# Performance work log

Measured on AMD Instinct MI355X. Metric: run time of the kernel, lower is better.

The kernel has to match this reference:

```python
import jax, jax.numpy as jnp
import numpy as np

DIM = 512
HEADS = 8
DH = DIM // HEADS          # 64
M = DIM // 2               # 256 landmarks
PINV_ITERS = 6
KERNEL = 33                # residual_conv_kernel (lucidrains default)
SCALE = DH ** -0.5
LN_EPS = 1e-5


def setup_inputs() -> dict:
    key = jax.random.key(0)
    ks = jax.random.split(key, 6)
    b, n = 4, 4096
    x = jax.random.normal(ks[0], (b, n, DIM), jnp.float32)
    ln_w = jnp.ones((DIM,), jnp.float32)
    ln_b = jnp.zeros((DIM,), jnp.float32)
    w_qkv = jax.random.normal(ks[1], (DIM, 3 * DIM), jnp.float32) / np.float32(np.sqrt(DIM))
    w_out = jax.random.normal(ks[2], (DIM, DIM), jnp.float32) / np.float32(np.sqrt(DIM))
    b_out = jnp.zeros((DIM,), jnp.float32)
    # depthwise Conv2d(heads, heads, (33,1), groups=heads, bias=False): OIHW = (8,1,33,1)
    conv_w = jax.random.normal(ks[3], (HEADS, 1, KERNEL, 1), jnp.float32) / np.float32(np.sqrt(KERNEL))
    # admin_torch.as_module(8): residual x*omega + f(x), omega learnable scalar init sqrt(8)
    omega = jnp.asarray(np.sqrt(8.0), jnp.float32)
    return dict(x=x, ln_w=ln_w, ln_b=ln_b, w_qkv=w_qkv, w_out=w_out,
                b_out=b_out, conv_w=conv_w, omega=omega)


def _layernorm(x, w, b):
    mu = x.mean(-1, keepdims=True)
    var = x.var(-1, keepdims=True)
    return (x - mu) * jax.lax.rsqrt(var + LN_EPS) * w + b


def _moore_penrose_pinv(x, iters):
    # Newton-Schulz iteration, exactly as lucidrains nystrom-attention
    abs_x = jnp.abs(x)
    col = abs_x.sum(-1)
    row = abs_x.sum(-2)
    z = jnp.swapaxes(x, -1, -2) / (jnp.max(col) * jnp.max(row))
    I = jnp.eye(x.shape[-1], dtype=x.dtype)
    for _ in range(iters):
        xz = x @ z
        z = 0.25 * z @ (13. * I - xz @ (15. * I - xz @ (7. * I - xz)))
    return z


def reference(x, ln_w, ln_b, w_qkv, w_out, b_out, conv_w, omega):
    b, n, _ = x.shape
    nx = _layernorm(x, ln_w, ln_b)
    qkv = nx @ w_qkv                                # [b, n, 3*dim]
    q, k, v = jnp.split(qkv, 3, axis=-1)
    to_heads = lambda t: t.reshape(b, n, HEADS, DH).transpose(0, 2, 1, 3)  # bhnd
    q = to_heads(q) * SCALE
    k = to_heads(k)
    v = to_heads(v)
    l = n // M                                      # tokens per landmark group
    q_l = q.reshape(b, HEADS, M, l, DH).mean(3)     # [b,h,m,d]
    k_l = k.reshape(b, HEADS, M, l, DH).mean(3)
    sim1 = jnp.einsum('bhid,bhjd->bhij', q, k_l)    # [b,h,n,m]
    sim2 = jnp.einsum('bhid,bhjd->bhij', q_l, k_l)  # [b,h,m,m]
    sim3 = jnp.einsum('bhid,bhjd->bhij', q_l, k)    # [b,h,m,n]
    a1 = jax.nn.softmax(sim1, -1)
    a2 = jax.nn.softmax(sim2, -1)
    a3 = jax.nn.softmax(sim3, -1)
    a2_inv = _moore_penrose_pinv(a2, PINV_ITERS)
    out = (a1 @ a2_inv) @ (a3 @ v)                  # [b,h,n,d]
    # residual depthwise conv along the sequence dim of v
    res = jax.lax.conv_general_dilated(
        v, conv_w, window_strides=(1, 1),
        padding=((KERNEL // 2, KERNEL // 2), (0, 0)),
        dimension_numbers=('NCHW', 'OIHW', 'NCHW'),
        feature_group_count=HEADS)
    out = out + res
    out = out.transpose(0, 2, 1, 3).reshape(b, n, HEADS * DH)
    out = out @ w_out + b_out                       # to_out (dropout is eval no-op)
    return x * omega + out                          # admin residual
```

## Files before the change

### kernel.cpp

```cpp
#include <hip/hip_runtime.h>
#include <math.h>

#define B_    4
#define N_    4096
#define DIM_  512
#define H_    8
#define DH_   64
#define M_    256
#define LGRP  16
#define BH_   (B_*H_)
#define SCALE_ 0.125f
#define LN_EPS_ 1e-5f

#define SZ_QKVH (B_*H_*N_*DH_)
#define SZ_LM   (BH_*M_*DH_)
#define SZ_MM   (BH_*M_*M_)

typedef unsigned short ushort_t;
typedef __attribute__((ext_vector_type(8))) short bfrag8;
typedef __attribute__((ext_vector_type(4))) float fvec4;

__device__ __forceinline__ ushort_t f2b(float f) {
    unsigned u = __float_as_uint(f);
    unsigned r = (u + 0x7fffu + ((u >> 16) & 1u)) >> 16;
    return (ushort_t)r;
}
__device__ __forceinline__ float b2f(ushort_t s) {
    return __uint_as_float(((unsigned)s) << 16);
}

__device__ __forceinline__ void gload16(const ushort_t* g, ushort_t* l) {
    __builtin_amdgcn_global_load_lds(
        (const __attribute__((address_space(1))) void*)g,
        (__attribute__((address_space(3))) void*)l, 16, 0, 0);
}

__global__ __launch_bounds__(256) void ln_kernel(const float* __restrict__ x,
                                                 const float* __restrict__ w,
                                                 const float* __restrict__ bb,
                                                 ushort_t* __restrict__ nxb) {
    int row = blockIdx.x;
    int t = threadIdx.x;
    const float* xr = x + (size_t)row * DIM_;
    float v0 = xr[t], v1 = xr[t + 256];
    float s = v0 + v1, sq = v0 * v0 + v1 * v1;
    __shared__ float ls[4], lq[4];
    for (int off = 32; off > 0; off >>= 1) {
        s  += __shfl_down(s, off);
        sq += __shfl_down(sq, off);
    }
    int wid = t >> 6, lid = t & 63;
    if (lid == 0) { ls[wid] = s; lq[wid] = sq; }
    __syncthreads();
    if (t == 0) {
        float S = 0, Q = 0;
        for (int i = 0; i < 4; i++) { S += ls[i]; Q += lq[i]; }
        ls[0] = S; lq[0] = Q;
    }
    __syncthreads();
    float mean = ls[0] * (1.f / DIM_);
    float var  = lq[0] * (1.f / DIM_) - mean * mean;
    float rs = rsqrtf(var + LN_EPS_);
    ushort_t* o = nxb + (size_t)row * DIM_;
    o[t]       = f2b((v0 - mean) * rs * w[t]       + bb[t]);
    o[t + 256] = f2b((v1 - mean) * rs * w[t + 256] + bb[t + 256]);
}

__global__ __launch_bounds__(256) void tcast(const float* __restrict__ in,
                                             ushort_t* __restrict__ outT,
                                             int R, int C) {
    __shared__ float tile[32][33];
    int c0 = blockIdx.x * 32, r0 = blockIdx.y * 32;
    int t = threadIdx.x;
    #pragma unroll
    for (int u = 0; u < 4; u++) {
        int lin = t + 256 * u;
        int r = lin >> 5, c = lin & 31;
        tile[r][c] = in[(size_t)(r0 + r) * C + c0 + c];
    }
    __syncthreads();
    #pragma unroll
    for (int u = 0; u < 4; u++) {
        int lin = t + 256 * u;
        int cc = lin >> 5, rr = lin & 31;
        outT[(size_t)(c0 + cc) * R + r0 + rr] = f2b(tile[rr][cc]);
    }
}

template<int EPI>
__global__ __launch_bounds__(256) void gemm_bt128(const ushort_t* __restrict__ A,
                                                  const ushort_t* __restrict__ BT,
                                                  ushort_t* __restrict__ qb,
                                                  ushort_t* __restrict__ kb,
                                                  ushort_t* __restrict__ vb,
                                                  const float* __restrict__ x,
                                                  const float* __restrict__ bo,
                                                  const float* __restrict__ omega,
                                                  float* __restrict__ out) {
    const int K = 512;
    __shared__ __align__(16) ushort_t smem[4 * 128 * 64];
    int t = threadIdx.x;
    int lin = blockIdx.x + blockIdx.y * gridDim.x;
    int nwg = gridDim.x * gridDim.y;
    int wg  = (lin & 7) * (nwg >> 3) + (lin >> 3);
    int n0 = (wg % gridDim.x) * 128, m0 = (wg / gridDim.x) * 128;
    int w = t >> 6, lane = t & 63;
    int wr = (w >> 1) * 64, wc = (w & 1) * 64;
    int l15 = lane & 15, quad = lane >> 4, kq = quad * 8;
    int lrow = lane >> 3, lc8 = (lane & 7) * 8;
    fvec4 acc[4][4] = {};

    auto stage = [&](int buf, int kc) {
        ushort_t* Ad = smem + buf * 16384;
        ushort_t* Bd = Ad + 8192;
        #pragma unroll
        for (int u = 0; u < 4; u++) {
            int r0 = (w << 5) + (u << 3);
            int row = r0 + lrow;
            const ushort_t* ga;
            if (EPI == 0) {
                ga = A + (size_t)(m0 + row) * K + kc + lc8;
            } else {
                int grow = m0 + row; int b_ = grow >> 12, nn = grow & 4095;
                ga = A + (((size_t)(b_ * H_ + (kc >> 6)) * N_ + nn) << 6) + lc8;
            }
            gload16(ga, Ad + r0 * 64);
            gload16(BT + (size_t)(n0 + row) * K + kc + lc8, Bd + r0 * 64);
        }
    };

    stage(0, 0);
    __syncthreads();
    int cur = 0;
    for (int kt = 0; kt < 8; ++kt) {
        if (kt < 7) stage(cur ^ 1, (kt + 1) * 64);
        const ushort_t* As = smem + cur * 16384;
        const ushort_t* Bs = As + 8192;
        #pragma unroll
        for (int ks = 0; ks < 64; ks += 32) {
            bfrag8 a[4], b[4];
            #pragma unroll
            for (int r = 0; r < 4; r++) a[r] = *(bfrag8*)(As + (wr + r * 16 + l15) * 64 + ks + kq);
            #pragma unroll
            for (int c = 0; c < 4; c++) b[c] = *(bfrag8*)(Bs + (wc + c * 16 + l15) * 64 + ks + kq);
            #pragma unroll
            for (int r = 0; r < 4; r++)
                #pragma unroll
                for (int c = 0; c < 4; c++)
                    acc[r][c] = __builtin_amdgcn_mfma_f32_16x16x32_bf16(a[r], b[c], acc[r][c], 0, 0, 0);
        }
        __syncthreads();
        cur ^= 1;
    }

    if (EPI == 0) {
        int sec = n0 >> 9;
        float mul = (sec == 0) ? SCALE_ : 1.0f;
        ushort_t (*Ct)[132] = (ushort_t(*)[132])smem;
        #pragma unroll
        for (int r = 0; r < 4; r++) {
            #pragma unroll
            for (int reg = 0; reg < 4; reg++) {
                int lr = wr + r * 16 + quad * 4 + reg;
                #pragma unroll
                for (int c = 0; c < 4; c++) {
                    int lc = wc + c * 16 + l15;
                    Ct[lr][lc] = f2b(acc[r][c][reg] * mul);
                }
            }
        }
        __syncthreads();
        int row = t & 127, half = t >> 7;
        int grow = m0 + row; int b_ = grow >> 12, nn = grow & 4095;
        int head = ((n0 & 511) >> 6) + half;
        ushort_t* dstbuf = (sec == 0) ? qb : ((sec == 1) ? kb : vb);
        ushort_t* dp = dstbuf + (((size_t)(b_ * H_ + head) * N_ + nn) << 6);
        #pragma unroll
        for (int i = 0; i < 8; i++)
            *(uint4*)(dp + i * 8) = *(uint4*)&Ct[row][half * 64 + i * 8];
    } else {
        float om = omega[0];
        #pragma unroll
        for (int r = 0; r < 4; r++) {
            #pragma unroll
            for (int reg = 0; reg < 4; reg++) {
                int grow = m0 + wr + r * 16 + quad * 4 + reg;
                #pragma unroll
                for (int c = 0; c < 4; c++) {
                    int gcol = n0 + wc + c * 16 + l15;
                    size_t o = (size_t)grow * DIM_ + gcol;
                    out[o] = om * x[o] + bo[gcol] + acc[r][c][reg];
                }
            }
        }
    }
}

__global__ __launch_bounds__(256) void landmark_kernel(const ushort_t* __restrict__ q,
                                                       const ushort_t* __restrict__ k,
                                                       ushort_t* __restrict__ ql,
                                                       ushort_t* __restrict__ kl) {
    int idx = blockIdx.x * 256 + threadIdx.x;
    const ushort_t* src = blockIdx.y ? k : q;
    ushort_t* dst = blockIdx.y ? kl : ql;
    int d8 = (idx & 7) * 8;
    int m = (idx >> 3) & 255;
    int bh = idx >> 11;
    const ushort_t* p = src + (((size_t)bh * N_) + m * LGRP) * DH_ + d8;
    float s[8] = {};
    #pragma unroll
    for (int j = 0; j < LGRP; j++) {
        union { uint4 u4; ushort_t sv[8]; } val;
        val.u4 = *(const uint4*)(p + (size_t)j * DH_);
        #pragma unroll
        for (int e = 0; e < 8; e++) s[e] += b2f(val.sv[e]);
    }
    union { uint4 u4; ushort_t sv[8]; } o;
    #pragma unroll
    for (int e = 0; e < 8; e++) o.sv[e] = f2b(s[e] * (1.f / LGRP));
    *(uint4*)(dst + ((size_t)bh * M_ + m) * DH_ + d8) = o.u4;
}

__global__ __launch_bounds__(256) void sim2_softmax(const ushort_t* __restrict__ ql,
                                                    const ushort_t* __restrict__ kl,
                                                    float* __restrict__ a2,
                                                    ushort_t* __restrict__ a2b) {
    int i = blockIdx.x, bh = blockIdx.y, j = threadIdx.x;
    __shared__ float qrow[64];
    __shared__ float red[256];
    if (j < 64) qrow[j] = b2f(ql[((size_t)bh * M_ + i) * DH_ + j]);
    __syncthreads();
    const ushort_t* kr = kl + ((size_t)bh * M_ + j) * DH_;
    float s = 0;
    #pragma unroll
    for (int d = 0; d < 64; d++) s += qrow[d] * b2f(kr[d]);
    red[j] = s; __syncthreads();
    for (int off = 128; off > 0; off >>= 1) {
        if (j < off) red[j] = fmaxf(red[j], red[j + off]);
        __syncthreads();
    }
    float mx = red[0]; __syncthreads();
    float p = __expf(s - mx);
    red[j] = p; __syncthreads();
    for (int off = 128; off > 0; off >>= 1) {
        if (j < off) red[j] += red[j + off];
        __syncthreads();
    }
    float res = p / red[0];
    size_t o = ((size_t)bh * M_ + i) * M_ + j;
    a2[o] = res;
    a2b[o] = f2b(res);
}

__global__ void zero2(unsigned* p) { if (threadIdx.x < 2) p[threadIdx.x] = 0u; }

__global__ __launch_bounds__(256) void colpart(const float* __restrict__ a2,
                                               float* __restrict__ cs2) {
    int bh = blockIdx.x, s = blockIdx.y, t = threadIdx.x;
    const float* A = a2 + ((size_t)bh << 16) + (size_t)s * 32 * M_;
    float cs = 0.f;
    #pragma unroll
    for (int i = 0; i < 32; i++) cs += A[(size_t)i * M_ + t];
    cs2[((size_t)s * BH_ + bh) * M_ + t] = cs;
}

__global__ __launch_bounds__(256) void colmax(const float* __restrict__ cs2, unsigned* red) {
    int bh = blockIdx.x, t = threadIdx.x;
    float v = 0.f;
    #pragma unroll
    for (int s = 0; s < 8; s++) v += cs2[((size_t)s * BH_ + bh) * M_ + t];
    __shared__ float lr[256];
    lr[t] = v; __syncthreads();
    for (int off = 128; off > 0; off >>= 1) {
        if (t < off) lr[t] = fmaxf(lr[t], lr[t + off]);
        __syncthreads();
    }
    if (t == 0) atomicMax(red, __float_as_uint(lr[0]));
}

__global__ __launch_bounds__(256) void pinv_init2(const float* __restrict__ a2,
                                                  const unsigned* __restrict__ red,
                                                  ushort_t* __restrict__ zA,
                                                  ushort_t* __restrict__ zAT) {
    __shared__ float tile[32][33];
    int bt = blockIdx.z; int j0 = blockIdx.x * 32, i0 = blockIdx.y * 32;
    float invd = 1.f / __uint_as_float(red[0]);
    const float* Ab = a2 + ((size_t)bt << 16);
    size_t bo = (size_t)bt << 16;
    int t = threadIdx.x;
    #pragma unroll
    for (int u = 0; u < 4; u++) {
        int lin = t + 256 * u; int r = lin >> 5, c = lin & 31;
        float vv = Ab[(size_t)(i0 + r) * M_ + j0 + c] * invd;
        tile[r][c] = vv;
        zAT[bo + (size_t)(i0 + r) * M_ + j0 + c] = f2b(vv);
    }
    __syncthreads();
    #pragma unroll
    for (int u = 0; u < 4; u++) {
        int lin = t + 256 * u; int cc = lin >> 5, rr = lin & 31;
        zA[bo + (size_t)(j0 + cc) * M_ + i0 + rr] = f2b(tile[rr][cc]);
    }
}

__global__ __launch_bounds__(256) void gemm_pinv(const ushort_t* __restrict__ A,
                                                 const ushort_t* __restrict__ BT,
                                                 ushort_t* __restrict__ outN,
                                                 ushort_t* __restrict__ outT,
                                                 ushort_t* __restrict__ outT1,
                                                 float* __restrict__ outF,
                                                 float coefI, float scale) {
    __shared__ __align__(16) ushort_t smem[2 * 8192];
    int t = threadIdx.x;
    int lin = blockIdx.x + (blockIdx.y << 2) + (blockIdx.z << 4);
    int wg  = (lin & 7) * 64 + (lin >> 3);
    int n0 = (wg & 3) * 64, m0 = ((wg >> 2) & 3) * 64;
    int bt = wg >> 4;
    const ushort_t* Ab = A + ((size_t)bt << 16);
    const ushort_t* Bb = BT + ((size_t)bt << 16);
    int w = t >> 6, lane = t & 63;
    int wr = (w >> 1) * 32, wc = (w & 1) * 32;
    int l15 = lane & 15, quad = lane >> 4, kq = quad * 8;
    int lrow = lane >> 3, lc8 = (lane & 7) * 8;
    fvec4 acc[2][2] = {};

    auto stage = [&](int buf, int kc) {
        ushort_t* Ad = smem + buf * 8192;
        ushort_t* Bd = Ad + 4096;
        #pragma unroll
        for (int u = 0; u < 2; u++) {
            int r0 = (w << 4) + (u << 3);
            int row = r0 + lrow;
            gload16(Ab + (size_t)(m0 + row) * M_ + kc + lc8, Ad + r0 * 64);
            gload16(Bb + (size_t)(n0 + row) * M_ + kc + lc8, Bd + r0 * 64);
        }
    };

    stage(0, 0);
    __syncthreads();
    int cur = 0;
    for (int kt = 0; kt < 4; ++kt) {
        if (kt < 3) stage(cur ^ 1, (kt + 1) * 64);
        const ushort_t* As = smem + cur * 8192;
        const ushort_t* Bs = As + 4096;
        #pragma unroll
        for (int ks = 0; ks < 64; ks += 32) {
            bfrag8 a[2], b[2];
            #pragma unroll
            for (int r = 0; r < 2; r++) a[r] = *(bfrag8*)(As + (wr + r * 16 + l15) * 64 + ks + kq);
            #pragma unroll
            for (int c = 0; c < 2; c++) b[c] = *(bfrag8*)(Bs + (wc + c * 16 + l15) * 64 + ks + kq);
            #pragma unroll
            for (int r = 0; r < 2; r++)
                #pragma unroll
                for (int c = 0; c < 2; c++)
                    acc[r][c] = __builtin_amdgcn_mfma_f32_16x16x32_bf16(a[r], b[c], acc[r][c], 0, 0, 0);
        }
        __syncthreads();
        cur ^= 1;
    }

    size_t bto = (size_t)bt << 16;
    if (outN || outF) {
        #pragma unroll
        for (int r = 0; r < 2; r++) {
            #pragma unroll
            for (int reg = 0; reg < 4; reg++) {
                int grow = m0 + wr + r * 16 + quad * 4 + reg;
                #pragma unroll
                for (int c = 0; c < 2; c++) {
                    int gcol = n0 + wc + c * 16 + l15;
                    float cv = scale * acc[r][c][reg] + (grow == gcol ? coefI : 0.f);
                    if (outN) outN[bto + (size_t)grow * M_ + gcol] = f2b(cv);
                    if (outF) outF[bto + (size_t)grow * M_ + gcol] = cv;
                }
            }
        }
    }
    if (outT || outT1) {
        ushort_t (*Ct)[65] = (ushort_t(*)[65])&smem[0];
        #pragma unroll
        for (int r = 0; r < 2; r++) {
            #pragma unroll
            for (int reg = 0; reg < 4; reg++) {
                int lr = wr + r * 16 + quad * 4 + reg;
                #pragma unroll
                for (int c = 0; c < 2; c++) {
                    int lc = wc + c * 16 + l15;
                    float cv = scale * acc[r][c][reg] + ((m0 + lr) == (n0 + lc) ? coefI : 0.f);
                    Ct[lr][lc] = f2b(cv);
                }
            }
        }
        __syncthreads();
        int j = t & 63, quarter = t >> 6, i0 = quarter * 16;
        #pragma unroll
        for (int vq = 0; vq < 2; vq++) {
            union { uint4 u4; ushort_t s[8]; } o1, o2;
            #pragma unroll
            for (int e = 0; e < 8; e++) {
                int il = i0 + vq * 8 + e;
                ushort_t bv = Ct[il][j];
                o1.s[e] = bv;
                o2.s[e] = f2b(((m0 + il) == (n0 + j) ? 7.f : 0.f) - b2f(bv));
            }
            size_t dst = bto + (size_t)(n0 + j) * M_ + m0 + i0 + vq * 8;
            if (outT)  *(uint4*)&outT[dst]  = o1.u4;
            if (outT1) *(uint4*)&outT1[dst] = o2.u4;
        }
    }
}

template<int NCH, int TRANSV>
__global__ __launch_bounds__(256) void flash_mfma(const ushort_t* __restrict__ Q,
                                                  const ushort_t* __restrict__ K,
                                                  const ushort_t* __restrict__ V,
                                                  ushort_t* __restrict__ Obf,
                                                  float* __restrict__ Opart,
                                                  float* __restrict__ lout,
                                                  int nq, int nk) {
    int bh = blockIdx.y;
    int nqt = nq >> 6;
    int qt = blockIdx.x % nqt;
    int ch = blockIdx.x / nqt;
    int q0 = qt * 64;
    int chunk = nk / NCH;
    int j0 = ch * chunk, j1 = j0 + chunk;

    __shared__ __align__(16) ushort_t qs[64][72];
    __shared__ __align__(16) ushort_t ks[64][72];
    __shared__ __align__(16) ushort_t vts[64][72];
    __shared__ __align__(16) ushort_t pb[64][72];

    int t = threadIdx.x;
    int w = t >> 6, lane = t & 63;
    int l15 = lane & 15, quad = lane >> 4, kq = quad * 8;
    int wrow = w * 16;

    const ushort_t* Qb = Q + ((size_t)bh * nq + q0) * DH_;
    #pragma unroll
    for (int u = 0; u < 2; u++) {
        int lin = t + 256 * u;
        int r = lin >> 3, cc = (lin & 7) * 8;
        *(uint4*)&qs[r][cc] = *(const uint4*)(Qb + r * DH_ + cc);
    }

    fvec4 Oacc[4];
    #pragma unroll
    for (int nt = 0; nt < 4; nt++)
        #pragma unroll
        for (int reg = 0; reg < 4; reg++) Oacc[nt][reg] = 0.f;
    float l_[4] = {0.f, 0.f, 0.f, 0.f};

    const ushort_t* VTbase = V + (size_t)bh * DH_ * nk;

    uint4 kreg[2], vreg[2];
    auto loadkv = [&](int j) {
        const ushort_t* Kb = K + ((size_t)bh * nk + j) * DH_;
        #pragma unroll
        for (int u = 0; u < 2; u++) {
            int lin = t + 256 * u;
            int r = lin >> 3, cc = (lin & 7) * 8;
            kreg[u] = *(const uint4*)(Kb + r * DH_ + cc);
            if (TRANSV == 0)
                vreg[u] = *(const uint4*)(VTbase + (size_t)r * nk + j + cc);
            else
                vreg[u] = *(const uint4*)(V + ((size_t)(bh * nk + j + r)) * DH_ + cc);
        }
    };
    auto writekv = [&]() {
        #pragma unroll
        for (int u = 0; u < 2; u++) {
            int lin = t + 256 * u;
            int r = lin >> 3, cc = (lin & 7) * 8;
            *(uint4*)&ks[r][cc] = kreg[u];
            if (TRANSV == 0) {
                *(uint4*)&vts[r][cc] = vreg[u];
            } else {
                union { uint4 u4; ushort_t s[8]; } vv;
                vv.u4 = vreg[u];
                #pragma unroll
                for (int m = 0; m < 8; m++) vts[cc + m][r] = vv.s[m];
            }
        }
    };

    loadkv(j0);
    for (int j = j0; j < j1; j += 64) {
        writekv();
        __syncthreads();
        if (j + 64 < j1) loadkv(j + 64);

        fvec4 S[4];
        #pragma unroll
        for (int ct = 0; ct < 4; ct++)
            #pragma unroll
            for (int reg = 0; reg < 4; reg++) S[ct][reg] = 0.f;
        bfrag8 aq0 = *(bfrag8*)&qs[wrow + l15][kq];
        bfrag8 aq1 = *(bfrag8*)&qs[wrow + l15][32 + kq];
        #pragma unroll
        for (int ct = 0; ct < 4; ct++) {
            bfrag8 b0 = *(bfrag8*)&ks[ct * 16 + l15][kq];
            bfrag8 b1 = *(bfrag8*)&ks[ct * 16 + l15][32 + kq];
            S[ct] = __builtin_amdgcn_mfma_f32_16x16x32_bf16(aq0, b0, S[ct], 0, 0, 0);
            S[ct] = __builtin_amdgcn_mfma_f32_16x16x32_bf16(aq1, b1, S[ct], 0, 0, 0);
        }

        float ps[4] = {0.f, 0.f, 0.f, 0.f};
        #pragma unroll
        for (int ct = 0; ct < 4; ct++) {
            #pragma unroll
            for (int reg = 0; reg < 4; reg++) {
                float pv = __expf(S[ct][reg]);
                ps[reg] += pv;
                pb[wrow + quad * 4 + reg][ct * 16 + l15] = f2b(pv);
            }
        }
        #pragma unroll
        for (int reg = 0; reg < 4; reg++) {
            float s = ps[reg];
            s += __shfl_xor(s, 1);
            s += __shfl_xor(s, 2);
            s += __shfl_xor(s, 4);
            s += __shfl_xor(s, 8);
            l_[reg] += s;
        }

        bfrag8 ap0 = *(bfrag8*)&pb[wrow + l15][kq];
        bfrag8 ap1 = *(bfrag8*)&pb[wrow + l15][32 + kq];
        #pragma unroll
        for (int nt = 0; nt < 4; nt++) {
            bfrag8 b0 = *(bfrag8*)&vts[nt * 16 + l15][kq];
            bfrag8 b1 = *(bfrag8*)&vts[nt * 16 + l15][32 + kq];
            Oacc[nt] = __builtin_amdgcn_mfma_f32_16x16x32_bf16(ap0, b0, Oacc[nt], 0, 0, 0);
            Oacc[nt] = __builtin_amdgcn_mfma_f32_16x16x32_bf16(ap1, b1, Oacc[nt], 0, 0, 0);
        }
        __syncthreads();
    }

    if (NCH == 1) {
        #pragma unroll
        for (int reg = 0; reg < 4; reg++) {
            float inv = 1.f / l_[reg];
            #pragma unroll
            for (int nt = 0; nt < 4; nt++)
                qs[wrow + quad * 4 + reg][nt * 16 + l15] = f2b(Oacc[nt][reg] * inv);
        }
        __syncthreads();
        ushort_t* Ob = Obf + ((size_t)bh * nq + q0) * DH_;
        #pragma unroll
        for (int u = 0; u < 2; u++) {
            int lin = t + 256 * u;
            int r = lin >> 3, i = (lin & 7) * 8;
            *(uint4*)(Ob + (size_t)r * DH_ + i) = *(uint4*)&qs[r][i];
        }
    } else {
        size_t rows_per_ch = (size_t)BH_ * nq;
        #pragma unroll
        for (int reg = 0; reg < 4; reg++) {
            size_t rowg = (size_t)bh * nq + q0 + wrow + quad * 4 + reg;
            #pragma unroll
            for (int nt = 0; nt < 4; nt++)
                Opart[((size_t)ch * rows_per_ch + rowg) * DH_ + nt * 16 + l15] = Oacc[nt][reg];
            if (l15 == 0)
                lout[(size_t)ch * rows_per_ch + rowg] = l_[reg];
        }
    }
}

__global__ __launch_bounds__(256) void flash_combine(const float* __restrict__ apart,
                                                     const float* __restrict__ lpart,
                                                     ushort_t* __restrict__ a3vb) {
    int idx = blockIdx.x * 256 + threadIdx.x;
    int d = idx & 63; int row = idx >> 6;
    const int R = BH_ * M_;
    float l = lpart[row] + lpart[row + R] + lpart[row + 2 * R] + lpart[row + 3 * R];
    size_t e = (size_t)row * DH_ + d;
    const size_t CH = (size_t)R * DH_;
    float o = apart[e] + apart[e + CH] + apart[e + 2 * CH] + apart[e + 3 * CH];
    a3vb[e] = f2b(o / l);
}

__global__ __launch_bounds__(256) void wm_mfma(const ushort_t* __restrict__ Z,
                                               const ushort_t* __restrict__ A3V,
                                               ushort_t* __restrict__ WmT) {
    __shared__ __align__(16) ushort_t As[64][72];
    __shared__ __align__(16) ushort_t Bs[64][72];
    int bh = blockIdx.y;
    int i0 = blockIdx.x * 64;
    const ushort_t* Zb = Z + ((size_t)bh << 16);
    const ushort_t* Ab = A3V + ((size_t)bh << 14);
    int t = threadIdx.x;
    int w = t >> 6, lane = t & 63;
    int wr = (w >> 1) * 32, wc = (w & 1) * 32;
    int l15 = lane & 15, quad = lane >> 4, kq = quad * 8;
    fvec4 acc[2][2] = {};
    int rbase = t >> 3, c8 = (t & 7) * 8;

    for (int kc = 0; kc < M_; kc += 64) {
        #pragma unroll
        for (int u = 0; u < 2; u++) {
            int rr = rbase + 32 * u;
            *(float4*)&Bs[rr][c8] = *(const float4*)(Zb + (size_t)(i0 + rr) * M_ + kc + c8);
            union { uint4 u4; ushort_t s[8]; } av;
            av.u4 = *(const uint4*)(Ab + (size_t)(kc + rr) * DH_ + c8);
            #pragma unroll
            for (int m = 0; m < 8; m++) As[c8 + m][rr] = av.s[m];
        }
        __syncthreads();
        #pragma unroll
        for (int ks = 0; ks < 64; ks += 32) {
            bfrag8 a[2], b[2];
            #pragma unroll
            for (int r = 0; r < 2; r++) a[r] = *(bfrag8*)&As[wr + r * 16 + l15][ks + kq];
            #pragma unroll
            for (int c = 0; c < 2; c++) b[c] = *(bfrag8*)&Bs[wc + c * 16 + l15][ks + kq];
            #pragma unroll
            for (int r = 0; r < 2; r++)
                #pragma unroll
                for (int c = 0; c < 2; c++)
                    acc[r][c] = __builtin_amdgcn_mfma_f32_16x16x32_bf16(a[r], b[c], acc[r][c], 0, 0, 0);
        }
        __syncthreads();
    }
    #pragma unroll
    for (int r = 0; r < 2; r++) {
        #pragma unroll
        for (int reg = 0; reg < 4; reg++) {
            int drow = wr + r * 16 + quad * 4 + reg;
            ushort_t* dp = WmT + ((size_t)bh * DH_ + drow) * M_;
            #pragma unroll
            for (int c = 0; c < 2; c++)
                dp[i0 + wc + c * 16 + l15] = f2b(acc[r][c][reg]);
        }
    }
}

__global__ __launch_bounds__(256) void conv_kernel(const ushort_t* __restrict__ V,
                                                   const float* __restrict__ cw,
                                                   const ushort_t* __restrict__ ctxb,
                                                   ushort_t* __restrict__ outb) {
    int bh = blockIdx.y;
    int h = bh & 7;
    int i0 = blockIdx.x * 64;
    __shared__ float vb[96][64];
    __shared__ float wloc[33];
    int t = threadIdx.x;
    if (t < 33) wloc[t] = cw[h * 33 + t];
    #pragma unroll
    for (int u = 0; u < 3; u++) {
        int lin = t + 256 * u;
        int r = lin >> 3, cc = (lin & 7) * 8;
        int gi = i0 - 16 + r;
        union { uint4 u4; ushort_t s[8]; } val;
        if (gi >= 0 && gi < N_)
            val.u4 = *(const uint4*)(V + ((size_t)bh * N_ + gi) * DH_ + cc);
        else
            val.u4 = make_uint4(0, 0, 0, 0);
        #pragma unroll
        for (int m = 0; m < 8; m++) vb[r][cc + m] = b2f(val.s[m]);
    }
    __syncthreads();
    int d = t & 63, rb = t >> 6;
    for (int u = 0; u < 16; u++) {
        int r = rb * 16 + u;
        float s = 0.f;
        #pragma unroll
        for (int kk = 0; kk < 33; kk++) s += wloc[kk] * vb[r + kk][d];
        size_t o = ((size_t)bh * N_ + i0 + r) * DH_ + d;
        outb[o] = f2b(b2f(ctxb[o]) + s);
    }
}

extern "C" void kernel_launch(void* const* d_in, const int* in_sizes, int n_in,
                              void* d_out, int out_size, void* d_ws, size_t ws_size,
                              hipStream_t stream) {
    const float* x      = (const float*)d_in[0];
    const float* ln_w   = (const float*)d_in[1];
    const float* ln_b   = (const float*)d_in[2];
    const float* w_qkv  = (const float*)d_in[3];
    const float* w_out  = (const float*)d_in[4];
    const float* b_out  = (const float*)d_in[5];
    const float* conv_w = (const float*)d_in[6];
    const float* omega  = (const float*)d_in[7];
    float* out = (float*)d_out;

    float* fp = (float*)d_ws;
    float* a2    = fp;              fp += SZ_MM;
    float* apart = fp;              fp += SZ_QKVH / 4;
    float* lpart = fp;              fp += 4 * BH_ * M_;
    float* cs2   = fp;              fp += 8 * BH_ * M_;
    ushort_t* us = (ushort_t*)fp;
    ushort_t* wqkvT = us;           us += DIM_ * 3 * DIM_;
    ushort_t* woT   = us;           us += DIM_ * DIM_;
    ushort_t* a2b   = us;           us += SZ_MM;
    ushort_t* zA    = us;           us += SZ_MM;
    ushort_t* zAT   = us;           us += SZ_MM;
    ushort_t* zB    = us;           us += SZ_MM;
    ushort_t* zBT   = us;           us += SZ_MM;
    ushort_t* qb    = us;           us += SZ_QKVH;
    ushort_t* kb    = us;           us += SZ_QKVH;
    ushort_t* vb    = us;           us += SZ_QKVH;
    ushort_t* ctxb  = us;           us += SZ_QKVH;
    ushort_t* outhb = us;           us += SZ_QKVH;
    ushort_t* ql    = us;           us += SZ_LM;
    ushort_t* kl    = us;           us += SZ_LM;
    ushort_t* WmT   = us;           us += SZ_LM;
    ushort_t* a3vb  = us;           us += SZ_LM;
    unsigned* red   = (unsigned*)us;
    ushort_t* nxb = outhb;
    ushort_t* xz  = ctxb;
    ushort_t* t1T = xz  + SZ_MM;
    ushort_t* t2T = t1T + SZ_MM;
    ushort_t* t3T = t2T + SZ_MM;

    ln_kernel<<<B_ * N_, 256, 0, stream>>>(x, ln_w, ln_b, nxb);
    tcast<<<dim3(48, 16), 256, 0, stream>>>(w_qkv, wqkvT, DIM_, 3 * DIM_);
    tcast<<<dim3(16, 16), 256, 0, stream>>>(w_out, woT, DIM_, DIM_);
    gemm_bt128<0><<<dim3(12, 128), 256, 0, stream>>>(nxb, wqkvT, qb, kb, vb,
                                                     nullptr, nullptr, nullptr, nullptr);
    landmark_kernel<<<dim3(256, 2), 256, 0, stream>>>(qb, kb, ql, kl);
    sim2_softmax<<<dim3(M_, BH_), 256, 0, stream>>>(ql, kl, a2, a2b);
    zero2<<<1, 64, 0, stream>>>(red);
    colpart<<<dim3(BH_, 8), 256, 0, stream>>>(a2, cs2);
    colmax<<<BH_, 256, 0, stream>>>(cs2, red);
    pinv_init2<<<dim3(8, 8, 32), 256, 0, stream>>>(a2, red, zA, zAT);

    ushort_t* za = zA;  ushort_t* zaT = zAT;
    ushort_t* zb = zB;  ushort_t* zbT = zBT;
    for (int it = 0; it < 6; it++) {
        gemm_pinv<<<dim3(4, 4, BH_), 256, 0, stream>>>(a2b, zaT, xz, nullptr, t1T, nullptr, 0.f, 1.f);
        gemm_pinv<<<dim3(4, 4, BH_), 256, 0, stream>>>(xz, t1T, nullptr, t2T, nullptr, nullptr, 15.f, -1.f);
        gemm_pinv<<<dim3(4, 4, BH_), 256, 0, stream>>>(xz, t2T, nullptr, t3T, nullptr, nullptr, 13.f, -1.f);
        gemm_pinv<<<dim3(4, 4, BH_), 256, 0, stream>>>(za, t3T, zb, (it < 5) ? zbT : nullptr,
                                                       nullptr, nullptr, 0.f, 0.25f);
        ushort_t* tp;
        tp = za; za = zb; zb = tp;
        tp = zaT; zaT = zbT; zbT = tp;
    }

    flash_mfma<4, 1><<<dim3(16, BH_), 256, 0, stream>>>(ql, kb, vb, nullptr, apart, lpart, M_, N_);
    flash_combine<<<(BH_ * M_ * DH_) / 256, 256, 0, stream>>>(apart, lpart, a3vb);
    wm_mfma<<<dim3(4, BH_), 256, 0, stream>>>(za, a3vb, WmT);
    flash_mfma<1, 0><<<dim3(64, BH_), 256, 0, stream>>>(qb, kl, WmT, ctxb, nullptr, nullptr, N_, M_);
    conv_kernel<<<dim3(N_ / 64, BH_), 256, 0, stream>>>(vb, conv_w, ctxb, outhb);
    gemm_bt128<1><<<dim3(4, 128), 256, 0, stream>>>(outhb, woT, nullptr, nullptr, nullptr,
                                                    x, b_out, omega, out);
}
```

Before: 500.8 us.

## Swizzle GEMM shared-memory tiles, double split-K chunks, stage partial outputs via LDS

Applies an XOR swizzle to the LDS layout of the QKV/out-projection and pinv GEMM tiles so MFMA fragment reads avoid bank conflicts. Raises the a3·v flash split count from 4 to 8 chunks to launch more workgroups for the short-query path, with the combine kernel summing 8 partials. Partial outputs are now staged through shared memory and written as coalesced float4 stores. The extra chunks double partial-buffer traffic and combine work.

```diff
diff --git a/kernel.cpp b/kernel.cpp
--- a/kernel.cpp
+++ b/kernel.cpp
@@ -108,6 +108,8 @@
     int wr = (w >> 1) * 64, wc = (w & 1) * 64;
     int l15 = lane & 15, quad = lane >> 4, kq = quad * 8;
     int lrow = lane >> 3, lc8 = (lane & 7) * 8;
+    int scol = lc8 ^ ((lrow & 7) << 3);
+    int sw   = (l15 & 7) << 3;
     fvec4 acc[4][4] = {};
 
     auto stage = [&](int buf, int kc) {
@@ -119,13 +121,13 @@
             int row = r0 + lrow;
             const ushort_t* ga;
             if (EPI == 0) {
-                ga = A + (size_t)(m0 + row) * K + kc + lc8;
+                ga = A + (size_t)(m0 + row) * K + kc + scol;
             } else {
                 int grow = m0 + row; int b_ = grow >> 12, nn = grow & 4095;
-                ga = A + (((size_t)(b_ * H_ + (kc >> 6)) * N_ + nn) << 6) + lc8;
+                ga = A + (((size_t)(b_ * H_ + (kc >> 6)) * N_ + nn) << 6) + scol;
             }
             gload16(ga, Ad + r0 * 64);
-            gload16(BT + (size_t)(n0 + row) * K + kc + lc8, Bd + r0 * 64);
+            gload16(BT + (size_t)(n0 + row) * K + kc + scol, Bd + r0 * 64);
         }
     };
 
@@ -138,11 +140,12 @@
         const ushort_t* Bs = As + 8192;
         #pragma unroll
         for (int ks = 0; ks < 64; ks += 32) {
+            int kcol = (ks + kq) ^ sw;
             bfrag8 a[4], b[4];
             #pragma unroll
-            for (int r = 0; r < 4; r++) a[r] = *(bfrag8*)(As + (wr + r * 16 + l15) * 64 + ks + kq);
-            #pragma unroll
-            for (int c = 0; c < 4; c++) b[c] = *(bfrag8*)(Bs + (wc + c * 16 + l15) * 64 + ks + kq);
+            for (int r = 0; r < 4; r++) a[r] = *(bfrag8*)(As + (wr + r * 16 + l15) * 64 + kcol);
+            #pragma unroll
+            for (int c = 0; c < 4; c++) b[c] = *(bfrag8*)(Bs + (wc + c * 16 + l15) * 64 + kcol);
             #pragma unroll
             for (int r = 0; r < 4; r++)
                 #pragma unroll
@@ -322,6 +325,8 @@
     int wr = (w >> 1) * 32, wc = (w & 1) * 32;
     int l15 = lane & 15, quad = lane >> 4, kq = quad * 8;
     int lrow = lane >> 3, lc8 = (lane & 7) * 8;
+    int scol = lc8 ^ ((lrow & 7) << 3);
+    int sw   = (l15 & 7) << 3;
     fvec4 acc[2][2] = {};
 
     auto stage = [&](int buf, int kc) {
@@ -331,8 +336,8 @@
         for (int u = 0; u < 2; u++) {
             int r0 = (w << 4) + (u << 3);
             int row = r0 + lrow;
-            gload16(Ab + (size_t)(m0 + row) * M_ + kc + lc8, Ad + r0 * 64);
-            gload16(Bb + (size_t)(n0 + row) * M_ + kc + lc8, Bd + r0 * 64);
+            gload16(Ab + (size_t)(m0 + row) * M_ + kc + scol, Ad + r0 * 64);
+            gload16(Bb + (size_t)(n0 + row) * M_ + kc + scol, Bd + r0 * 64);
         }
     };
 
@@ -345,11 +350,12 @@
         const ushort_t* Bs = As + 4096;
         #pragma unroll
         for (int ks = 0; ks < 64; ks += 32) {
+            int kcol = (ks + kq) ^ sw;
             bfrag8 a[2], b[2];
             #pragma unroll
-            for (int r = 0; r < 2; r++) a[r] = *(bfrag8*)(As + (wr + r * 16 + l15) * 64 + ks + kq);
-            #pragma unroll
-            for (int c = 0; c < 2; c++) b[c] = *(bfrag8*)(Bs + (wc + c * 16 + l15) * 64 + ks + kq);
+            for (int r = 0; r < 2; r++) a[r] = *(bfrag8*)(As + (wr + r * 16 + l15) * 64 + kcol);
+            #pragma unroll
+            for (int c = 0; c < 2; c++) b[c] = *(bfrag8*)(Bs + (wc + c * 16 + l15) * 64 + kcol);
             #pragma unroll
             for (int r = 0; r < 2; r++)
                 #pragma unroll
@@ -555,15 +561,27 @@
             *(uint4*)(Ob + (size_t)r * DH_ + i) = *(uint4*)&qs[r][i];
         }
     } else {
+        float (*Of)[68] = (float(*)[68])&ks[0][0];
+        #pragma unroll
+        for (int reg = 0; reg < 4; reg++)
+            #pragma unroll
+            for (int nt = 0; nt < 4; nt++)
+                Of[wrow + quad * 4 + reg][nt * 16 + l15] = Oacc[nt][reg];
         size_t rows_per_ch = (size_t)BH_ * nq;
-        #pragma unroll
-        for (int reg = 0; reg < 4; reg++) {
-            size_t rowg = (size_t)bh * nq + q0 + wrow + quad * 4 + reg;
-            #pragma unroll
-            for (int nt = 0; nt < 4; nt++)
-                Opart[((size_t)ch * rows_per_ch + rowg) * DH_ + nt * 16 + l15] = Oacc[nt][reg];
-            if (l15 == 0)
-                lout[(size_t)ch * rows_per_ch + rowg] = l_[reg];
+        size_t rowbase = (size_t)ch * rows_per_ch + (size_t)bh * nq + q0;
+        if (l15 == 0) {
+            #pragma unroll
+            for (int reg = 0; reg < 4; reg++)
+                lout[rowbase + wrow + quad * 4 + reg] = l_[reg];
+        }
+        __syncthreads();
+        int orow = t >> 2, oc = (t & 3) * 16;
+        float* Od = Opart + (rowbase + orow) * DH_ + oc;
+        #pragma unroll
+        for (int i = 0; i < 4; i++) {
+            float4 v4 = make_float4(Of[orow][oc + i * 4], Of[orow][oc + i * 4 + 1],
+                                    Of[orow][oc + i * 4 + 2], Of[orow][oc + i * 4 + 3]);
+            *(float4*)(Od + i * 4) = v4;
         }
     }
 }
@@ -574,10 +592,14 @@
     int idx = blockIdx.x * 256 + threadIdx.x;
     int d = idx & 63; int row = idx >> 6;
     const int R = BH_ * M_;
-    float l = lpart[row] + lpart[row + R] + lpart[row + 2 * R] + lpart[row + 3 * R];
     size_t e = (size_t)row * DH_ + d;
     const size_t CH = (size_t)R * DH_;
-    float o = apart[e] + apart[e + CH] + apart[e + 2 * CH] + apart[e + 3 * CH];
+    float l = 0.f, o = 0.f;
+    #pragma unroll
+    for (int s = 0; s < 8; s++) {
+        l += lpart[row + (size_t)s * R];
+        o += apart[e + (size_t)s * CH];
+    }
     a3vb[e] = f2b(o / l);
 }
 
@@ -687,8 +709,8 @@
 
     float* fp = (float*)d_ws;
     float* a2    = fp;              fp += SZ_MM;
-    float* apart = fp;              fp += SZ_QKVH / 4;
-    float* lpart = fp;              fp += 4 * BH_ * M_;
+    float* apart = fp;              fp += SZ_QKVH / 2;
+    float* lpart = fp;              fp += 8 * BH_ * M_;
     float* cs2   = fp;              fp += 8 * BH_ * M_;
     ushort_t* us = (ushort_t*)fp;
     ushort_t* wqkvT = us;           us += DIM_ * 3 * DIM_;
@@ -739,7 +761,7 @@
         tp = zaT; zaT = zbT; zbT = tp;
     }
 
-    flash_mfma<4, 1><<<dim3(16, BH_), 256, 0, stream>>>(ql, kb, vb, nullptr, apart, lpart, M_, N_);
+    flash_mfma<8, 1><<<dim3(32, BH_), 256, 0, stream>>>(ql, kb, vb, nullptr, apart, lpart, M_, N_);
     flash_combine<<<(BH_ * M_ * DH_) / 256, 256, 0, stream>>>(apart, lpart, a3vb);
     wm_mfma<<<dim3(4, BH_), 256, 0, stream>>>(za, a3vb, WmT);
     flash_mfma<1, 0><<<dim3(64, BH_), 256, 0, stream>>>(qb, kl, WmT, ctxb, nullptr, nullptr, N_, M_);
```

Result: no change. 501.3 us (+0.1%).
